# Optimization experiments

Hardware: AMD Instinct MI355X
Metric: run time of the kernel (lower is better)

## Reference

```python
import jax, jax.numpy as jnp
import numpy as np


def setup_inputs() -> dict:
    key = jax.random.key(0)
    k1, k2 = jax.random.split(key)
    N, M, C = 8192, 16384, 128
    features = jax.random.normal(k1, (N, 1, 1, C), dtype=jnp.float32)
    patch_memory = jax.random.normal(k2, (1, M, 1, C), dtype=jnp.float32)
    return {"features": features, "patch_memory": patch_memory}


def reference(features, patch_memory):
    # Faithful to: torch.norm(features - patch_memory, dim=3); torch.min(dim=1)
    # features: [N, 1, 1, C], patch_memory: [1, M, 1, C] -> broadcast diff [N, M, 1, C]
    # Avoid materializing the [N, M, C] diff tensor: use the GEMM expansion
    # ||a-b||^2 = ||a||^2 + ||b||^2 - 2 a.b (same math, efficient form).
    f = features.reshape(features.shape[0], features.shape[-1])       # [N, C]
    m = patch_memory.reshape(patch_memory.shape[1], patch_memory.shape[-1])  # [M, C]
    f2 = jnp.sum(f * f, axis=-1)   # [N]
    m2 = jnp.sum(m * m, axis=-1)   # [M]
    cross = jnp.einsum('nc,mc->nm', f, m)  # [N, M]
    d2 = f2[:, None] + m2[None, :] - 2.0 * cross
    distances = jnp.sqrt(jnp.maximum(d2, 0.0))       # [N, M] == norm over dim 3
    min_distances = jnp.min(distances, axis=1)       # min over memory dim (dim=1)
    # original keeps the trailing singleton patch dim -> [N, 1]
    return min_distances[:, None]
```

## Files before the change

### kernel.cpp

```cpp
#include <hip/hip_runtime.h>
#include <hip/hip_bf16.h>
#include <stdint.h>

#define N_ROWS 8192
#define M_ROWS 16384
#define CDIM 128
#define MSPLIT 4
#define NT 32
#define BTR 128
#define TILE_U16 (BTR * CDIM)

typedef unsigned short u16;
typedef __attribute__((ext_vector_type(8))) short bf16x8;
typedef __attribute__((ext_vector_type(16))) float f32x16;

static __device__ __forceinline__ u16 f2bf(float x) {
  union { float f; uint32_t u; } v; v.f = x;
  uint32_t u = v.u;
  uint32_t r = u + 0x7FFFu + ((u >> 16) & 1u);
  return (u16)(r >> 16);
}
static __device__ __forceinline__ float bf2f(u16 b) {
  union { uint32_t u; float f; } v; v.u = ((uint32_t)b) << 16;
  return v.f;
}

#define GLOAD_LDS(gsrc, ldst)                                                  \
  __builtin_amdgcn_global_load_lds(                                            \
      (const __attribute__((address_space(1))) uint32_t*)(gsrc),               \
      (__attribute__((address_space(3))) uint32_t*)(ldst), 16, 0, 0)

__global__ __launch_bounds__(256) void prep_kernel(
    const float* __restrict__ f, const float* __restrict__ m,
    u16* __restrict__ fb, u16* __restrict__ mb,
    float* __restrict__ f2, float* __restrict__ mh, int* __restrict__ mind2)
{
  const int row = blockIdx.x * 4 + (threadIdx.x >> 6);
  const int lane = threadIdx.x & 63;
  const bool isF = row < N_ROWS;
  const int r = isF ? row : row - N_ROWS;
  const float* src = (isF ? f : m) + (size_t)r * CDIM;
  float2 v = *(const float2*)(src + lane * 2);
  u16 b0 = f2bf(v.x), b1 = f2bf(v.y);
  float x0 = bf2f(b0), x1 = bf2f(b1);
  float s = x0 * x0 + x1 * x1;
#pragma unroll
  for (int mask = 1; mask < 64; mask <<= 1)
    s += __shfl_xor(s, mask, 64);

  const int t = r >> 5, lr = r & 31;
  const int ks = lane >> 3;
  const int l5p = (lane >> 2) & 1;
  const int j = (lane & 3) * 2;
  u16* dst = (isF ? fb : mb)
             + ((size_t)(t * 8 + ks) * 64 + l5p * 32 + lr) * 8 + j;
  dst[0] = b0; dst[1] = b1;
  if (lane == 0) {
    if (isF) { f2[r] = s; mind2[r] = 0x7F7FFFFF; }
    else     { mh[r] = -0.5f * s; }
  }
}

__global__ __launch_bounds__(512, 2) void gemm_min_kernel(
    const u16* __restrict__ fb, const u16* __restrict__ mb,
    const float* __restrict__ f2, const float* __restrict__ mh,
    int* __restrict__ mind2)
{
  __shared__ __align__(16) u16 bts[3 * TILE_U16];
  __shared__ __align__(16) float mhl[4096];
  const int tid = threadIdx.x;
  const int lane = tid & 63;
  const int w = tid >> 6;
  const int wm = w >> 2;
  const int wn = w & 3;
  const int l31 = lane & 31;
  const int l5 = lane >> 5;
  const int abase = blockIdx.y * 128;
  const size_t mslice = (size_t)blockIdx.x * 4096;

  bf16x8 af[2][8];
#pragma unroll
  for (int mi = 0; mi < 2; ++mi) {
    const int ta = (abase >> 5) + wm * 2 + mi;
#pragma unroll
    for (int ks = 0; ks < 8; ++ks)
      af[mi][ks] = *(const bf16x8*)&fb[((size_t)(ta * 8 + ks) * 64 + lane) * 8];
  }

  const float* mhsrc = mh + mslice;
#pragma unroll
  for (int c = 0; c < 2; ++c) {
    const int c16 = c * 512 + tid;
    GLOAD_LDS(mhsrc + c16 * 4, mhl + c16 * 4);
  }
  const u16* mbase_ptr = mb + mslice * CDIM;
#pragma unroll
  for (int tt = 0; tt < 2; ++tt)
#pragma unroll
    for (int c = 0; c < 4; ++c) {
      const int t16 = c * 512 + tid;
      GLOAD_LDS(mbase_ptr + (size_t)tt * TILE_U16 + t16 * 8,
                bts + tt * TILE_U16 + t16 * 8);
    }
  asm volatile("s_waitcnt vmcnt(4)" ::: "memory");
  __builtin_amdgcn_s_barrier();

  float tmax[2][16];
#pragma unroll
  for (int mi = 0; mi < 2; ++mi)
#pragma unroll
    for (int r = 0; r < 16; ++r) tmax[mi][r] = -3.0e38f;

  f32x16 accA[2], accB[2];
#pragma unroll
  for (int mi = 0; mi < 2; ++mi)
#pragma unroll
    for (int r = 0; r < 16; ++r) accB[mi][r] = -3.0e38f;

  const int wnoff = wn * (8 * 64 * 8);
  int c0 = 0;

  for (int t = 0; t < NT; t += 2) {
    int c1 = c0 + 1; if (c1 >= 3) c1 -= 3;
    int c2 = c0 + 2; if (c2 >= 3) c2 -= 3;

    {
      const u16* bt = bts + c0 * TILE_U16 + wnoff;
      bf16x8 bg[8];
#pragma unroll
      for (int ks = 0; ks < 8; ++ks)
        bg[ks] = *(const bf16x8*)&bt[((size_t)ks * 64 + lane) * 8];
      const float mhA = mhl[t * BTR + wn * 32 + l31];
      {
        const u16* srcT = mbase_ptr + (size_t)((t + 2) & (NT - 1)) * TILE_U16;
        u16* dstT = bts + c2 * TILE_U16;
#pragma unroll
        for (int c = 0; c < 4; ++c) {
          const int t16 = c * 512 + tid;
          GLOAD_LDS(srcT + t16 * 8, dstT + t16 * 8);
        }
      }
      asm volatile("s_waitcnt vmcnt(4)" ::: "memory");
      __builtin_amdgcn_s_barrier();

#pragma unroll
      for (int mi = 0; mi < 2; ++mi)
#pragma unroll
        for (int r = 0; r < 16; ++r) accA[mi][r] = mhA;
      __builtin_amdgcn_s_setprio(1);
#pragma unroll
      for (int ks = 0; ks < 8; ++ks)
#pragma unroll
        for (int mi = 0; mi < 2; ++mi)
          accA[mi] = __builtin_amdgcn_mfma_f32_32x32x16_bf16(
              af[mi][ks], bg[ks], accA[mi], 0, 0, 0);
      __builtin_amdgcn_s_setprio(0);
#pragma unroll
      for (int mi = 0; mi < 2; ++mi)
#pragma unroll
        for (int r = 0; r < 16; ++r)
          tmax[mi][r] = fmaxf(tmax[mi][r], accB[mi][r]);
    }

    {
      const u16* bt = bts + c1 * TILE_U16 + wnoff;
      bf16x8 bg[8];
#pragma unroll
      for (int ks = 0; ks < 8; ++ks)
        bg[ks] = *(const bf16x8*)&bt[((size_t)ks * 64 + lane) * 8];
      const float mhB = mhl[(t + 1) * BTR + wn * 32 + l31];
      {
        const u16* srcT = mbase_ptr + (size_t)((t + 3) & (NT - 1)) * TILE_U16;
        u16* dstT = bts + c0 * TILE_U16;
#pragma unroll
        for (int c = 0; c < 4; ++c) {
          const int t16 = c * 512 + tid;
          GLOAD_LDS(srcT + t16 * 8, dstT + t16 * 8);
        }
      }
      asm volatile("s_waitcnt vmcnt(4)" ::: "memory");
      __builtin_amdgcn_s_barrier();

#pragma unroll
      for (int mi = 0; mi < 2; ++mi)
#pragma unroll
        for (int r = 0; r < 16; ++r) accB[mi][r] = mhB;
      __builtin_amdgcn_s_setprio(1);
#pragma unroll
      for (int ks = 0; ks < 8; ++ks)
#pragma unroll
        for (int mi = 0; mi < 2; ++mi)
          accB[mi] = __builtin_amdgcn_mfma_f32_32x32x16_bf16(
              af[mi][ks], bg[ks], accB[mi], 0, 0, 0);
      __builtin_amdgcn_s_setprio(0);
#pragma unroll
      for (int mi = 0; mi < 2; ++mi)
#pragma unroll
        for (int r = 0; r < 16; ++r)
          tmax[mi][r] = fmaxf(tmax[mi][r], accA[mi][r]);
    }
    c0 = c2;
  }
#pragma unroll
  for (int mi = 0; mi < 2; ++mi)
#pragma unroll
    for (int r = 0; r < 16; ++r)
      tmax[mi][r] = fmaxf(tmax[mi][r], accB[mi][r]);

#pragma unroll
  for (int mi = 0; mi < 2; ++mi)
#pragma unroll
    for (int r = 0; r < 16; ++r) {
      float tv = tmax[mi][r];
      tv = fmaxf(tv, __shfl_xor(tv, 1, 64));
      tv = fmaxf(tv, __shfl_xor(tv, 2, 64));
      tv = fmaxf(tv, __shfl_xor(tv, 4, 64));
      tv = fmaxf(tv, __shfl_xor(tv, 8, 64));
      tv = fmaxf(tv, __shfl_xor(tv, 16, 64));
      tmax[mi][r] = tv;
    }
  if (l31 == 0) {
#pragma unroll
    for (int mi = 0; mi < 2; ++mi)
#pragma unroll
      for (int r = 0; r < 16; ++r) {
        const int row = abase + wm * 64 + mi * 32
                        + (r & 3) + 8 * (r >> 2) + 4 * l5;
        const float d2 = fmaxf(fmaf(-2.0f, tmax[mi][r], f2[row]), 0.0f);
        atomicMin(&mind2[row], __float_as_int(d2));
      }
  }
}

__global__ __launch_bounds__(256) void finalize_kernel(
    const int* __restrict__ mind2, float* __restrict__ out)
{
  const int i = blockIdx.x * 256 + threadIdx.x;
  out[i] = sqrtf(fmaxf(__int_as_float(mind2[i]), 0.0f));
}

extern "C" void kernel_launch(void* const* d_in, const int* in_sizes, int n_in,
                              void* d_out, int out_size, void* d_ws, size_t ws_size,
                              hipStream_t stream) {
  const float* f = (const float*)d_in[0];
  const float* m = (const float*)d_in[1];

  char* ws = (char*)d_ws;
  u16*  fb    = (u16*)(ws);
  u16*  mb    = (u16*)(ws + (2u << 20));
  float* f2   = (float*)(ws + (2u << 20) + (4u << 20));
  float* mh   = (float*)(ws + (2u << 20) + (4u << 20) + (32u << 10));
  int*  mind2 = (int*)(ws + (2u << 20) + (4u << 20) + (96u << 10));

  hipLaunchKernelGGL(prep_kernel, dim3((N_ROWS + M_ROWS) / 4), dim3(256), 0, stream,
                     f, m, fb, mb, f2, mh, mind2);
  hipLaunchKernelGGL(gemm_min_kernel, dim3(MSPLIT, N_ROWS / 128), dim3(512), 0, stream,
                     fb, mb, f2, mh, mind2);
  hipLaunchKernelGGL(finalize_kernel, dim3(N_ROWS / 256), dim3(256), 0, stream,
                     mind2, (float*)d_out);
}
```

Before: 52.31 us.

## Prefetch next B tile fragments into registers and use 4-stage LDS ring

Register-prefetches the next tile's B fragments and mh value from LDS before the current tile's MFMA chain, so LDS read latency overlaps matrix compute. The LDS ring grows from 3 to 4 tile buffers so a slot is not overwritten while its fragments are still being read. Buffer indices become power-of-two masks instead of modular counters. This costs more LDS (which may hurt the 2-blocks-per-CU occupancy) and more VGPRs for the doubled bg arrays.

```diff
diff --git a/kernel.cpp b/kernel.cpp
--- a/kernel.cpp
+++ b/kernel.cpp
@@ -66,7 +66,7 @@
     const float* __restrict__ f2, const float* __restrict__ mh,
     int* __restrict__ mind2)
 {
-  __shared__ __align__(16) u16 bts[3 * TILE_U16];
+  __shared__ __align__(16) u16 bts[4 * TILE_U16];
   __shared__ __align__(16) float mhl[4096];
   const int tid = threadIdx.x;
   const int lane = tid & 63;
@@ -77,6 +77,7 @@
   const int l5 = lane >> 5;
   const int abase = blockIdx.y * 128;
   const size_t mslice = (size_t)blockIdx.x * 4096;
+  const int mhbase = wn * 32 + l31;
 
   bf16x8 af[2][8];
 #pragma unroll
@@ -105,6 +106,19 @@
   asm volatile("s_waitcnt vmcnt(4)" ::: "memory");
   __builtin_amdgcn_s_barrier();
 
+  const int wnoff = wn * (8 * 64 * 8);
+  const int rdoff = lane * 8;
+
+  bf16x8 bgA[8], bgB[8];
+  float mhA, mhB;
+  {
+    const u16* bt = bts + wnoff;
+#pragma unroll
+    for (int ks = 0; ks < 8; ++ks)
+      bgA[ks] = *(const bf16x8*)&bt[ks * (64 * 8) + rdoff];
+    mhA = mhl[mhbase];
+  }
+
   float tmax[2][16];
 #pragma unroll
   for (int mi = 0; mi < 2; ++mi)
@@ -117,32 +131,24 @@
 #pragma unroll
     for (int r = 0; r < 16; ++r) accB[mi][r] = -3.0e38f;
 
-  const int wnoff = wn * (8 * 64 * 8);
-  int c0 = 0;
-
   for (int t = 0; t < NT; t += 2) {
-    int c1 = c0 + 1; if (c1 >= 3) c1 -= 3;
-    int c2 = c0 + 2; if (c2 >= 3) c2 -= 3;
-
     {
-      const u16* bt = bts + c0 * TILE_U16 + wnoff;
-      bf16x8 bg[8];
-#pragma unroll
-      for (int ks = 0; ks < 8; ++ks)
-        bg[ks] = *(const bf16x8*)&bt[((size_t)ks * 64 + lane) * 8];
-      const float mhA = mhl[t * BTR + wn * 32 + l31];
-      {
-        const u16* srcT = mbase_ptr + (size_t)((t + 2) & (NT - 1)) * TILE_U16;
-        u16* dstT = bts + c2 * TILE_U16;
-#pragma unroll
-        for (int c = 0; c < 4; ++c) {
-          const int t16 = c * 512 + tid;
-          GLOAD_LDS(srcT + t16 * 8, dstT + t16 * 8);
-        }
+      const u16* srcT = mbase_ptr + (size_t)((t + 2) & (NT - 1)) * TILE_U16;
+      u16* dstT = bts + ((t + 2) & 3) * TILE_U16;
+#pragma unroll
+      for (int c = 0; c < 4; ++c) {
+        const int t16 = c * 512 + tid;
+        GLOAD_LDS(srcT + t16 * 8, dstT + t16 * 8);
       }
       asm volatile("s_waitcnt vmcnt(4)" ::: "memory");
       __builtin_amdgcn_s_barrier();
 
+      const u16* btn = bts + ((t + 1) & 3) * TILE_U16 + wnoff;
+#pragma unroll
+      for (int ks = 0; ks < 8; ++ks)
+        bgB[ks] = *(const bf16x8*)&btn[ks * (64 * 8) + rdoff];
+      mhB = mhl[((t + 1) & (NT - 1)) * BTR + mhbase];
+
 #pragma unroll
       for (int mi = 0; mi < 2; ++mi)
 #pragma unroll
@@ -153,7 +159,7 @@
 #pragma unroll
         for (int mi = 0; mi < 2; ++mi)
           accA[mi] = __builtin_amdgcn_mfma_f32_32x32x16_bf16(
-              af[mi][ks], bg[ks], accA[mi], 0, 0, 0);
+              af[mi][ks], bgA[ks], accA[mi], 0, 0, 0);
       __builtin_amdgcn_s_setprio(0);
 #pragma unroll
       for (int mi = 0; mi < 2; ++mi)
@@ -161,26 +167,23 @@
         for (int r = 0; r < 16; ++r)
           tmax[mi][r] = fmaxf(tmax[mi][r], accB[mi][r]);
     }
-
     {
-      const u16* bt = bts + c1 * TILE_U16 + wnoff;
-      bf16x8 bg[8];
-#pragma unroll
-      for (int ks = 0; ks < 8; ++ks)
-        bg[ks] = *(const bf16x8*)&bt[((size_t)ks * 64 + lane) * 8];
-      const float mhB = mhl[(t + 1) * BTR + wn * 32 + l31];
-      {
-        const u16* srcT = mbase_ptr + (size_t)((t + 3) & (NT - 1)) * TILE_U16;
-        u16* dstT = bts + c0 * TILE_U16;
-#pragma unroll
-        for (int c = 0; c < 4; ++c) {
-          const int t16 = c * 512 + tid;
-          GLOAD_LDS(srcT + t16 * 8, dstT + t16 * 8);
-        }
+      const u16* srcT = mbase_ptr + (size_t)((t + 3) & (NT - 1)) * TILE_U16;
+      u16* dstT = bts + ((t + 3) & 3) * TILE_U16;
+#pragma unroll
+      for (int c = 0; c < 4; ++c) {
+        const int t16 = c * 512 + tid;
+        GLOAD_LDS(srcT + t16 * 8, dstT + t16 * 8);
       }
       asm volatile("s_waitcnt vmcnt(4)" ::: "memory");
       __builtin_amdgcn_s_barrier();
 
+      const u16* btn = bts + ((t + 2) & 3) * TILE_U16 + wnoff;
+#pragma unroll
+      for (int ks = 0; ks < 8; ++ks)
+        bgA[ks] = *(const bf16x8*)&btn[ks * (64 * 8) + rdoff];
+      mhA = mhl[((t + 2) & (NT - 1)) * BTR + mhbase];
+
 #pragma unroll
       for (int mi = 0; mi < 2; ++mi)
 #pragma unroll
@@ -191,7 +194,7 @@
 #pragma unroll
         for (int mi = 0; mi < 2; ++mi)
           accB[mi] = __builtin_amdgcn_mfma_f32_32x32x16_bf16(
-              af[mi][ks], bg[ks], accB[mi], 0, 0, 0);
+              af[mi][ks], bgB[ks], accB[mi], 0, 0, 0);
       __builtin_amdgcn_s_setprio(0);
 #pragma unroll
       for (int mi = 0; mi < 2; ++mi)
@@ -199,7 +202,6 @@
         for (int r = 0; r < 16; ++r)
           tmax[mi][r] = fmaxf(tmax[mi][r], accA[mi][r]);
     }
-    c0 = c2;
   }
 #pragma unroll
   for (int mi = 0; mi < 2; ++mi)
```

Result: slower. 82.14 us (+57.0%).
